# Kernel tuning notes

Measured on AMD Instinct MI355X. Metric: run time of the kernel, lower is better.

## Reference

```python
import jax, jax.numpy as jnp
import numpy as np

B, D, NCLS = 65536, 784, 10

def sparse_layer(x, idx, w, b):
    # x: [B, D]; idx: [Dout, k] int; w: [Dout, k]; b: [Dout]
    # out[b, n] = sum_j x[b, idx[n, j]] * w[n, j] + b[n]
    g = x[:, idx]                      # [B, Dout, k] gather
    return jnp.einsum('bnk,nk->bn', g, w) + b

def setup_inputs() -> dict:
    key = jax.random.key(0)
    ks = jax.random.split(key, 12)
    def rn(k, shape, scale):
        return jax.random.normal(k, shape, dtype=jnp.float32) * scale
    return {
        'x': rn(ks[0], (B, D), 1.0),
        'idx1': jax.random.randint(ks[1], (D, 2), 0, D, dtype=jnp.int32),
        'w1': rn(ks[2], (D, 2), 0.5),
        'b1': rn(ks[3], (D,), 0.1),
        'idx2': jax.random.randint(ks[4], (D, 4), 0, D, dtype=jnp.int32),
        'w2': rn(ks[5], (D, 4), 0.4),
        'b2': rn(ks[6], (D,), 0.1),
        'idx3': jax.random.randint(ks[7], (D, 8), 0, D, dtype=jnp.int32),
        'w3': rn(ks[8], (D, 8), 0.3),
        'b3': rn(ks[9], (D,), 0.1),
        'fc_w': rn(ks[10], (NCLS, D), 0.05),
        'fc_b': rn(ks[11], (NCLS,), 0.05),
    }

def reference(x, idx1, w1, b1, idx2, w2, b2, idx3, w3, b3, fc_w, fc_b):
    h = jax.nn.gelu(sparse_layer(x, idx1, w1, b1), approximate=False)
    h = jax.nn.gelu(sparse_layer(h, idx2, w2, b2), approximate=False)
    h = jax.nn.gelu(sparse_layer(h, idx3, w3, b3), approximate=False)
    logits = h @ fc_w.T + fc_b          # [B, 10]
    return jax.nn.softmax(logits, axis=-1)
```

## Files before the change

kernel.cpp:

```cpp
#include <hip/hip_runtime.h>

#define D_    784
#define ROWS  8
#define NCLS  10
#define BLOCK 512
#define NB    (65536 / ROWS)
#define NPG   4

__device__ __forceinline__ float gelu_f(float x) {
    float x2    = x * x;
    float inner = fmaf(0.044715f * x, x2, x);
    float e     = exp2f(2.3022082f * inner);
    float r     = __builtin_amdgcn_rcpf(e + 1.0f);
    return fmaf(-x, r, x);
}

__device__ __forceinline__ void fma4(float4& a, const float4& h4, float wk) {
    a.x = fmaf(h4.x, wk, a.x);
    a.y = fmaf(h4.y, wk, a.y);
    a.z = fmaf(h4.z, wk, a.z);
    a.w = fmaf(h4.w, wk, a.w);
}

template <int K>
__device__ __forceinline__ void loadIdxW(const int* __restrict__ idx,
                                         const float* __restrict__ w,
                                         int n, int* jc, float* wc) {
    if constexpr (K == 2) {
        int2   j = *(const int2*)(idx + n * 2);
        float2 v = *(const float2*)(w + n * 2);
        jc[0] = j.x; jc[1] = j.y; wc[0] = v.x; wc[1] = v.y;
    } else if constexpr (K == 4) {
        int4   j = *(const int4*)(idx + n * 4);
        float4 v = *(const float4*)(w + n * 4);
        jc[0] = j.x; jc[1] = j.y; jc[2] = j.z; jc[3] = j.w;
        wc[0] = v.x; wc[1] = v.y; wc[2] = v.z; wc[3] = v.w;
    } else {
        int4   ja = *(const int4*)(idx + n * 8);
        int4   jb = *(const int4*)(idx + n * 8 + 4);
        float4 va = *(const float4*)(w + n * 8);
        float4 vb = *(const float4*)(w + n * 8 + 4);
        jc[0] = ja.x; jc[1] = ja.y; jc[2] = ja.z; jc[3] = ja.w;
        jc[4] = jb.x; jc[5] = jb.y; jc[6] = jb.z; jc[7] = jb.w;
        wc[0] = va.x; wc[1] = va.y; wc[2] = va.z; wc[3] = va.w;
        wc[4] = vb.x; wc[5] = vb.y; wc[6] = vb.z; wc[7] = vb.w;
    }
}

template <int K>
__device__ __forceinline__ void layer_fn(const float* __restrict__ src,
                                         float* __restrict__ dst,
                                         const int* __restrict__ idx,
                                         const float* __restrict__ w,
                                         const float* __restrict__ bias,
                                         int g, int q) {
    int   jc[K];
    float wc[K];
    float bc;
    loadIdxW<K>(idx, w, g, jc, wc);
    bc = bias[g];
#pragma unroll 1
    for (int i = 0; i < NPG; ++i) {
        int n  = g + 256 * i;
        int nn = n + 256;
        int   jn[K]; float wn[K]; float bn = 0.f;
#pragma unroll
        for (int k = 0; k < K; ++k) { jn[k] = 0; wn[k] = 0.f; }
        if (nn < D_) {
            loadIdxW<K>(idx, w, nn, jn, wn);
            bn = bias[nn];
        }
        if (n < D_) {
            float4 a = make_float4(bc, bc, bc, bc);
#pragma unroll
            for (int k = 0; k < K; ++k) {
                float4 hv = *(const float4*)(src + jc[k] * 8 + q * 4);
                fma4(a, hv, wc[k]);
            }
            *(float4*)(dst + n * 8 + q * 4) =
                make_float4(gelu_f(a.x), gelu_f(a.y), gelu_f(a.z), gelu_f(a.w));
        }
#pragma unroll
        for (int k = 0; k < K; ++k) { jc[k] = jn[k]; wc[k] = wn[k]; }
        bc = bn;
    }
    __syncthreads();
}

__global__ __launch_bounds__(BLOCK)
void circnn_kernel(const float* __restrict__ x,
                   const int* __restrict__ idx1, const float* __restrict__ w1, const float* __restrict__ b1,
                   const int* __restrict__ idx2, const float* __restrict__ w2, const float* __restrict__ b2,
                   const int* __restrict__ idx3, const float* __restrict__ w3, const float* __restrict__ b3,
                   const float* __restrict__ fcw, const float* __restrict__ fcb,
                   float* __restrict__ out) {
    __shared__ __align__(16) float bufA[D_ * ROWS];
    __shared__ __align__(16) float bufB[D_ * ROWS];
    __shared__ float logits[ROWS * NCLS];

    const int tid  = threadIdx.x;
    const int g    = tid >> 1;
    const int q    = tid & 1;
    const int row0 = blockIdx.x * ROWS;

    const float* xb = x + (size_t)row0 * D_;
#pragma unroll
    for (int c2 = 0; c2 < 2; ++c2) {
#pragma unroll 1
        for (int n = tid; n < D_; n += BLOCK) {
            float4 v;
            v.x = xb[(c2 * 4 + 0) * D_ + n];
            v.y = xb[(c2 * 4 + 1) * D_ + n];
            v.z = xb[(c2 * 4 + 2) * D_ + n];
            v.w = xb[(c2 * 4 + 3) * D_ + n];
            *(float4*)(bufA + n * 8 + c2 * 4) = v;
        }
    }
    __syncthreads();

    layer_fn<2>(bufA, bufB, idx1, w1, b1, g, q);
    layer_fn<4>(bufB, bufA, idx2, w2, b2, g, q);
    layer_fn<8>(bufA, bufB, idx3, w3, b3, g, q);

    float4* part4 = (float4*)bufA;
    if (tid < 128) {
        const int jj = tid >> 1;
        const int qq = tid & 1;
        float4 facc[NCLS];
#pragma unroll
        for (int c = 0; c < NCLS; ++c) facc[c] = make_float4(0.f, 0.f, 0.f, 0.f);
#pragma unroll 1
        for (int i = 0; i < 13; ++i) {
            int n = jj + 64 * i;
            if (n < D_) {
                float4 hv = *(const float4*)(bufB + n * 8 + qq * 4);
#pragma unroll
                for (int c = 0; c < NCLS; ++c)
                    fma4(facc[c], hv, fcw[c * D_ + n]);
            }
        }
#pragma unroll
        for (int c = 0; c < NCLS; ++c)
            part4[(jj * 2 + qq) * NCLS + c] = facc[c];
    }
    __syncthreads();

    if (tid < ROWS * NCLS) {
        int r = tid / NCLS, c = tid - r * NCLS;
        int qq = r >> 2, comp = r & 3;
        const float* pf = (const float*)part4;
        float s = fcb[c];
#pragma unroll 4
        for (int jj = 0; jj < 64; ++jj)
            s += pf[((jj * 2 + qq) * NCLS + c) * 4 + comp];
        logits[tid] = s;
    }
    __syncthreads();

    if (tid < ROWS * NCLS) {
        int r = tid / NCLS;
        const float* lg = logits + r * NCLS;
        float m = lg[0];
#pragma unroll
        for (int c = 1; c < NCLS; ++c) m = fmaxf(m, lg[c]);
        float s = 0.f;
#pragma unroll
        for (int c = 0; c < NCLS; ++c) s += __expf(lg[c] - m);
        out[(size_t)row0 * NCLS + tid] = __expf(logits[tid] - m) / s;
    }
}

extern "C" void kernel_launch(void* const* d_in, const int* in_sizes, int n_in,
                              void* d_out, int out_size, void* d_ws, size_t ws_size,
                              hipStream_t stream) {
    const float* x    = (const float*)d_in[0];
    const int*   idx1 = (const int*)d_in[1];
    const float* w1   = (const float*)d_in[2];
    const float* b1   = (const float*)d_in[3];
    const int*   idx2 = (const int*)d_in[4];
    const float* w2   = (const float*)d_in[5];
    const float* b2   = (const float*)d_in[6];
    const int*   idx3 = (const int*)d_in[7];
    const float* w3   = (const float*)d_in[8];
    const float* b3   = (const float*)d_in[9];
    const float* fcw  = (const float*)d_in[10];
    const float* fcb  = (const float*)d_in[11];
    float* out = (float*)d_out;

    circnn_kernel<<<dim3(NB), dim3(BLOCK), 0, stream>>>(
        x, idx1, w1, b1, idx2, w2, b2, idx3, w3, b3, fcw, fcb, out);
}
```

Baseline: 437.0 us.

## Halve block size, one thread per neuron over 8 rows, pad LDS stride

After: 486.0 us. 1.11x slower.

```diff
diff --git a/kernel.cpp b/kernel.cpp
--- a/kernel.cpp
+++ b/kernel.cpp
@@ -3,9 +3,9 @@
 #define D_    784
 #define ROWS  8
 #define NCLS  10
-#define BLOCK 512
+#define BLOCK 256
 #define NB    (65536 / ROWS)
-#define NPG   4
+#define HSTR  12
 
 __device__ __forceinline__ float gelu_f(float x) {
     float x2    = x * x;
@@ -53,15 +53,15 @@
                                          const int* __restrict__ idx,
                                          const float* __restrict__ w,
                                          const float* __restrict__ bias,
-                                         int g, int q) {
+                                         int tid) {
     int   jc[K];
     float wc[K];
     float bc;
-    loadIdxW<K>(idx, w, g, jc, wc);
-    bc = bias[g];
+    loadIdxW<K>(idx, w, tid, jc, wc);
+    bc = bias[tid];
 #pragma unroll 1
-    for (int i = 0; i < NPG; ++i) {
-        int n  = g + 256 * i;
+    for (int i = 0; i < 4; ++i) {
+        int n  = tid + 256 * i;
         int nn = n + 256;
         int   jn[K]; float wn[K]; float bn = 0.f;
 #pragma unroll
@@ -71,14 +71,21 @@
             bn = bias[nn];
         }
         if (n < D_) {
-            float4 a = make_float4(bc, bc, bc, bc);
+            float4 aL = make_float4(bc, bc, bc, bc);
+            float4 aH = make_float4(bc, bc, bc, bc);
 #pragma unroll
             for (int k = 0; k < K; ++k) {
-                float4 hv = *(const float4*)(src + jc[k] * 8 + q * 4);
-                fma4(a, hv, wc[k]);
+                const float* hb = src + jc[k] * HSTR;
+                float4 h0 = *(const float4*)(hb);
+                float4 h1 = *(const float4*)(hb + 4);
+                fma4(aL, h0, wc[k]);
+                fma4(aH, h1, wc[k]);
             }
-            *(float4*)(dst + n * 8 + q * 4) =
-                make_float4(gelu_f(a.x), gelu_f(a.y), gelu_f(a.z), gelu_f(a.w));
+            float* db = dst + n * HSTR;
+            *(float4*)(db)     = make_float4(gelu_f(aL.x), gelu_f(aL.y),
+                                             gelu_f(aL.z), gelu_f(aL.w));
+            *(float4*)(db + 4) = make_float4(gelu_f(aH.x), gelu_f(aH.y),
+                                             gelu_f(aH.z), gelu_f(aH.w));
         }
 #pragma unroll
         for (int k = 0; k < K; ++k) { jc[k] = jn[k]; wc[k] = wn[k]; }
@@ -94,33 +101,33 @@
                    const int* __restrict__ idx3, const float* __restrict__ w3, const float* __restrict__ b3,
                    const float* __restrict__ fcw, const float* __restrict__ fcb,
                    float* __restrict__ out) {
-    __shared__ __align__(16) float bufA[D_ * ROWS];
-    __shared__ __align__(16) float bufB[D_ * ROWS];
+    __shared__ __align__(16) float bufA[D_ * HSTR];
+    __shared__ __align__(16) float bufB[D_ * HSTR];
     __shared__ float logits[ROWS * NCLS];
 
     const int tid  = threadIdx.x;
-    const int g    = tid >> 1;
-    const int q    = tid & 1;
     const int row0 = blockIdx.x * ROWS;
 
     const float* xb = x + (size_t)row0 * D_;
-#pragma unroll
-    for (int c2 = 0; c2 < 2; ++c2) {
 #pragma unroll 1
-        for (int n = tid; n < D_; n += BLOCK) {
-            float4 v;
-            v.x = xb[(c2 * 4 + 0) * D_ + n];
-            v.y = xb[(c2 * 4 + 1) * D_ + n];
-            v.z = xb[(c2 * 4 + 2) * D_ + n];
-            v.w = xb[(c2 * 4 + 3) * D_ + n];
-            *(float4*)(bufA + n * 8 + c2 * 4) = v;
+    for (int i = 0; i < 4; ++i) {
+        int n = tid + 256 * i;
+        if (n < D_) {
+            float4 v0, v1;
+            v0.x = xb[0 * D_ + n]; v0.y = xb[1 * D_ + n];
+            v0.z = xb[2 * D_ + n]; v0.w = xb[3 * D_ + n];
+            v1.x = xb[4 * D_ + n]; v1.y = xb[5 * D_ + n];
+            v1.z = xb[6 * D_ + n]; v1.w = xb[7 * D_ + n];
+            float* db = bufA + n * HSTR;
+            *(float4*)(db)     = v0;
+            *(float4*)(db + 4) = v1;
         }
     }
     __syncthreads();
 
-    layer_fn<2>(bufA, bufB, idx1, w1, b1, g, q);
-    layer_fn<4>(bufB, bufA, idx2, w2, b2, g, q);
-    layer_fn<8>(bufA, bufB, idx3, w3, b3, g, q);
+    layer_fn<2>(bufA, bufB, idx1, w1, b1, tid);
+    layer_fn<4>(bufB, bufA, idx2, w2, b2, tid);
+    layer_fn<8>(bufA, bufB, idx3, w3, b3, tid);
 
     float4* part4 = (float4*)bufA;
     if (tid < 128) {
@@ -133,7 +140,7 @@
         for (int i = 0; i < 13; ++i) {
             int n = jj + 64 * i;
             if (n < D_) {
-                float4 hv = *(const float4*)(bufB + n * 8 + qq * 4);
+                float4 hv = *(const float4*)(bufB + n * HSTR + qq * 4);
 #pragma unroll
                 for (int c = 0; c < NCLS; ++c)
                     fma4(facc[c], hv, fcw[c * D_ + n]);
```
